# Optimization experiments

Hardware: AMD Instinct MI355X
Metric: run time of the kernel (lower is better)

Reference implementation:

```python
import jax, jax.numpy as jnp
import numpy as np

B, C, L, T = 8, 512, 2048, 64

def setup_inputs() -> dict:
    key = jax.random.key(0)
    k1, k2, k3 = jax.random.split(key, 3)
    x = jax.random.normal(k1, (B, C, 1, L), dtype=jnp.float32)
    W1 = jax.random.normal(k2, (T, C), dtype=jnp.float32) * (1.0 / np.sqrt(C))
    W2 = jax.random.normal(k3, (T, C), dtype=jnp.float32) * (1.0 / np.sqrt(C))
    gamma = jnp.ones((1, 1), dtype=jnp.float32)
    ranges = 0  # unused by forward
    return {"x": x, "W1": W1, "W2": W2, "gamma": gamma, "ranges": ranges}

def reference(x, W1, W2, gamma, ranges):
    temp = x[:, :, 0, :]                                  # (B, C, L)
    q = jnp.einsum('tc,bcl->btl', W1, temp)               # conv1x1 -> (B, T, L)
    k = jnp.einsum('tc,bcl->btl', W2, temp)               # conv1x1 -> (B, T, L)
    scores = jnp.einsum('btl,btm->blm', q, k)             # Q^T K -> (B, L, L)
    attn = jax.nn.softmax(scores, axis=2)                 # softmax over last dim
    # temp @ attn^T: out[:, :, j] = sum_i attn[j, i] * temp[:, :, i]
    out = jnp.einsum('bci,bji->bcj', temp, attn)          # (B, C, L)
    out = temp + gamma[0, 0] * out                        # gamma scale + residual
    return out[:, :, None, :]                             # (B, C, 1, L)
```

## Files before the change

### kernel.cpp

```cpp
#include <hip/hip_runtime.h>
#include <cstddef>

#define BB 8
#define CC 512
#define LL 2048
#define TT 64

typedef short short8 __attribute__((ext_vector_type(8)));
typedef float floatx4 __attribute__((ext_vector_type(4)));
typedef unsigned short b16u;
typedef unsigned int u32;

static __device__ __forceinline__ unsigned f2bfu(float f) {
    unsigned u = __float_as_uint(f);
    u += 0x7fffu + ((u >> 16) & 1u);
    return u >> 16;
}
static __device__ __forceinline__ float bfu2f(unsigned h) {
    return __uint_as_float(h << 16);
}

#define MFMA16(a, b, c) __builtin_amdgcn_mfma_f32_16x16x32_bf16((a), (b), (c), 0, 0, 0)

static __device__ __forceinline__ void gl2lds16(const void* g, void* l) {
    __builtin_amdgcn_global_load_lds(
        (const __attribute__((address_space(1))) u32*)g,
        (__attribute__((address_space(3))) u32*)l, 16, 0, 0);
}

__global__ __launch_bounds__(256) void wcvt_kernel(
    const float* __restrict__ W1, const float* __restrict__ W2,
    b16u* __restrict__ W1h, b16u* __restrict__ W1l,
    b16u* __restrict__ W2h, b16u* __restrict__ W2l)
{
    int flat = blockIdx.x * 256 + threadIdx.x;
    float4 v1 = *(const float4*)(W1 + (size_t)flat * 4);
    float4 v2 = *(const float4*)(W2 + (size_t)flat * 4);
    const float* e1 = (const float*)&v1;
    const float* e2 = (const float*)&v2;
    unsigned h1[4], l1[4], h2[4], l2[4];
#pragma unroll
    for (int k = 0; k < 4; ++k) {
        h1[k] = f2bfu(e1[k]); l1[k] = f2bfu(e1[k] - bfu2f(h1[k]));
        h2[k] = f2bfu(e2[k]); l2[k] = f2bfu(e2[k] - bfu2f(h2[k]));
    }
    uint2 a, b, c, d;
    a.x = h1[0] | (h1[1] << 16); a.y = h1[2] | (h1[3] << 16);
    b.x = l1[0] | (l1[1] << 16); b.y = l1[2] | (l1[3] << 16);
    c.x = h2[0] | (h2[1] << 16); c.y = h2[2] | (h2[3] << 16);
    d.x = l2[0] | (l2[1] << 16); d.y = l2[2] | (l2[3] << 16);
    *(uint2*)(W1h + (size_t)flat * 4) = a;
    *(uint2*)(W1l + (size_t)flat * 4) = b;
    *(uint2*)(W2h + (size_t)flat * 4) = c;
    *(uint2*)(W2l + (size_t)flat * 4) = d;
}

__global__ __launch_bounds__(256) void qkcvt_kernel(
    const float* __restrict__ x,
    const b16u* __restrict__ W1h, const b16u* __restrict__ W1l,
    const b16u* __restrict__ W2h, const b16u* __restrict__ W2l,
    b16u* __restrict__ Qt, b16u* __restrict__ Kt)
{
    __shared__ b16u Sxh[64 * 72];
    __shared__ b16u Sxl[64 * 72];
    __shared__ b16u S1h[64 * 72];
    __shared__ b16u S1l[64 * 72];
    __shared__ b16u S2h[64 * 72];
    __shared__ b16u S2l[64 * 72];
    const int b  = blockIdx.y;
    const int l0 = blockIdx.x * 64;
    const int tid = threadIdx.x;
    const int lane = tid & 63;
    const int w = tid >> 6;
    const int n16 = lane & 15;
    const int qd = lane >> 4;
    const float* xb = x + (size_t)b * CC * LL;

    const int cx = tid >> 2;
    const int sx = tid & 3;

    float4 xreg[4];
#pragma unroll
    for (int p = 0; p < 4; ++p)
        xreg[p] = *(const float4*)(xb + (size_t)cx * LL + l0 + (sx * 4 + p) * 4);

    floatx4 aq[4], ak[4];
#pragma unroll
    for (int nt = 0; nt < 4; ++nt) {
        aq[nt] = (floatx4){0.f, 0.f, 0.f, 0.f};
        ak[nt] = (floatx4){0.f, 0.f, 0.f, 0.f};
    }

    for (int c0 = 0; c0 < 512; c0 += 64) {
        __syncthreads();
#pragma unroll
        for (int p = 0; p < 4; ++p) {
            const float* e = (const float*)&xreg[p];
            int lbase = (sx * 4 + p) * 4;
#pragma unroll
            for (int k = 0; k < 4; ++k) {
                unsigned h = f2bfu(e[k]);
                unsigned lo = f2bfu(e[k] - bfu2f(h));
                Sxh[(lbase + k) * 72 + cx] = (b16u)h;
                Sxl[(lbase + k) * 72 + cx] = (b16u)lo;
            }
        }
#pragma unroll
        for (int p = 0; p < 2; ++p) {
            int flat = tid + p * 256;
            int t = flat >> 3, s8 = flat & 7;
            size_t off = (size_t)t * 512 + c0 + s8 * 8;
            *(uint4*)&S1h[t * 72 + s8 * 8] = *(const uint4*)(W1h + off);
            *(uint4*)&S1l[t * 72 + s8 * 8] = *(const uint4*)(W1l + off);
            *(uint4*)&S2h[t * 72 + s8 * 8] = *(const uint4*)(W2h + off);
            *(uint4*)&S2l[t * 72 + s8 * 8] = *(const uint4*)(W2l + off);
        }
        __syncthreads();
        if (c0 < 448) {
#pragma unroll
            for (int p = 0; p < 4; ++p)
                xreg[p] = *(const float4*)(xb + (size_t)(c0 + 64 + cx) * LL +
                                           l0 + (sx * 4 + p) * 4);
        }
#pragma unroll
        for (int kc = 0; kc < 2; ++kc) {
            const int ao = (w * 16 + n16) * 72 + kc * 32 + qd * 8;
            short8 a1h = *(const short8*)&S1h[ao];
            short8 a1l = *(const short8*)&S1l[ao];
            short8 a2h = *(const short8*)&S2h[ao];
            short8 a2l = *(const short8*)&S2l[ao];
#pragma unroll
            for (int nt = 0; nt < 4; ++nt) {
                const int bo = (nt * 16 + n16) * 72 + kc * 32 + qd * 8;
                short8 bh = *(const short8*)&Sxh[bo];
                short8 bl = *(const short8*)&Sxl[bo];
                aq[nt] = MFMA16(a1h, bh, aq[nt]);
                aq[nt] = MFMA16(a1h, bl, aq[nt]);
                aq[nt] = MFMA16(a1l, bh, aq[nt]);
                ak[nt] = MFMA16(a2h, bh, ak[nt]);
                ak[nt] = MFMA16(a2h, bl, ak[nt]);
                ak[nt] = MFMA16(a2l, bh, ak[nt]);
            }
        }
    }
#pragma unroll
    for (int nt = 0; nt < 4; ++nt) {
        int l = l0 + nt * 16 + n16;
        uint2 pq, pk;
        pq.x = f2bfu(aq[nt][0]) | (f2bfu(aq[nt][1]) << 16);
        pq.y = f2bfu(aq[nt][2]) | (f2bfu(aq[nt][3]) << 16);
        pk.x = f2bfu(ak[nt][0]) | (f2bfu(ak[nt][1]) << 16);
        pk.y = f2bfu(ak[nt][2]) | (f2bfu(ak[nt][3]) << 16);
        *(uint2*)(Qt + ((size_t)(b * 2048) + l) * 64 + w * 16 + qd * 4) = pq;
        *(uint2*)(Kt + ((size_t)(b * 2048) + l) * 64 + w * 16 + qd * 4) = pk;
    }
}

__global__ __launch_bounds__(256) void xcvt_kernel(
    const float* __restrict__ x, b16u* __restrict__ XT)
{
    const int b = blockIdx.z, c0 = blockIdx.y * 64, it = blockIdx.x;
    const int tid = threadIdx.x;
#pragma unroll
    for (int p = 0; p < 4; ++p) {
        int flat = tid + p * 256;
        int c = flat >> 4, s = flat & 15;
        float4 v = *(const float4*)(x + ((size_t)(b * 512) + c0 + c) * 2048 + it * 64 + s * 4);
        uint2 wv;
        wv.x = f2bfu(v.x) | (f2bfu(v.y) << 16);
        wv.y = f2bfu(v.z) | (f2bfu(v.w) << 16);
        int phys = (((s >> 1) ^ (c & 7)) << 3) + ((s & 1) << 2);
        *(uint2*)(XT + (((size_t)(b * 32) + it) * 512 + c0 + c) * 64 + phys) = wv;
    }
}

__global__ __launch_bounds__(256) void pexp_kernel(
    const b16u* __restrict__ Qt, const b16u* __restrict__ Kt,
    b16u* __restrict__ P, float* __restrict__ Zpart, int b_off)
{
    __shared__ b16u Ks[64 * 72];
    __shared__ b16u Ls[64 * 68];
    __shared__ float Zw[4][64];
    const int pb = blockIdx.z, b = b_off + pb;
    const int j0 = blockIdx.y * 64;
    const int ibase = blockIdx.x * 1024;
    const int tid = threadIdx.x;
    const int lane = tid & 63;
    const int w = tid >> 6;
    const int n16 = lane & 15;
    const int qd = lane >> 4;
    const b16u* kb = Kt + (size_t)b * (2048 * 64);

    short8 qf[4][2];
#pragma unroll
    for (int nt = 0; nt < 4; ++nt)
#pragma unroll
        for (int kc = 0; kc < 2; ++kc)
            qf[nt][kc] = *(const short8*)(Qt +
                ((size_t)(b * 2048) + j0 + nt * 16 + n16) * 64 + kc * 32 + qd * 8);

    uint4 kreg[2];
#pragma unroll
    for (int p = 0; p < 2; ++p) {
        int flat = tid + p * 256;
        kreg[p] = *(const uint4*)(kb + (size_t)(ibase + (flat >> 3)) * 64 + (flat & 7) * 8);
    }
    float zacc[4] = {0.f, 0.f, 0.f, 0.f};

    for (int it = 0; it < 16; ++it) {
#pragma unroll
        for (int p = 0; p < 2; ++p) {
            int flat = tid + p * 256;
            *(uint4*)&Ks[(flat >> 3) * 72 + (flat & 7) * 8] = kreg[p];
        }
        {
            const int itn = (it + 1 < 16) ? it + 1 : 15;
#pragma unroll
            for (int p = 0; p < 2; ++p) {
                int flat = tid + p * 256;
                kreg[p] = *(const uint4*)(kb +
                    (size_t)(ibase + itn * 64 + (flat >> 3)) * 64 + (flat & 7) * 8);
            }
        }
        __syncthreads();
        floatx4 sacc[4];
#pragma unroll
        for (int nt = 0; nt < 4; ++nt) sacc[nt] = (floatx4){0.f, 0.f, 0.f, 0.f};
#pragma unroll
        for (int kc = 0; kc < 2; ++kc) {
            short8 af = *(const short8*)&Ks[(w * 16 + n16) * 72 + kc * 32 + qd * 8];
#pragma unroll
            for (int nt = 0; nt < 4; ++nt)
                sacc[nt] = MFMA16(af, qf[nt][kc], sacc[nt]);
        }
#pragma unroll
        for (int nt = 0; nt < 4; ++nt) {
            float p0 = __expf(sacc[nt][0] - 20.0f);
            float p1 = __expf(sacc[nt][1] - 20.0f);
            float p2 = __expf(sacc[nt][2] - 20.0f);
            float p3 = __expf(sacc[nt][3] - 20.0f);
            zacc[nt] += (p0 + p1) + (p2 + p3);
            uint2 pk;
            pk.x = f2bfu(p0) | (f2bfu(p1) << 16);
            pk.y = f2bfu(p2) | (f2bfu(p3) << 16);
            *(uint2*)&Ls[(nt * 16 + n16) * 68 + w * 16 + qd * 4] = pk;
        }
        __syncthreads();
        size_t prow = ((size_t)(pb * 32) + (ibase >> 6) + it) * 2048 + j0;
#pragma unroll
        for (int p = 0; p < 4; ++p) {
            int u = tid + p * 256;
            int row = u >> 4, s = u & 15;
            int phys = (((s >> 1) ^ (row & 7)) << 3) + ((s & 1) << 2);
            *(uint2*)(P + (prow + row) * 64 + phys) = *(const uint2*)&Ls[row * 68 + s * 4];
        }
    }
#pragma unroll
    for (int nt = 0; nt < 4; ++nt) {
        float z = zacc[nt];
        z += __shfl_xor(z, 16);
        z += __shfl_xor(z, 32);
        if (qd == 0) Zw[w][nt * 16 + n16] = z;
    }
    __syncthreads();
    if (tid < 64) {
        float s = Zw[0][tid] + Zw[1][tid] + Zw[2][tid] + Zw[3][tid];
        Zpart[((size_t)blockIdx.x * 8 + b) * 2048 + j0 + tid] = s;
    }
}

__global__ __launch_bounds__(256, 2) void gemm_kernel(
    const float* __restrict__ x, const b16u* __restrict__ XT,
    const b16u* __restrict__ P, const float* __restrict__ Zpart,
    const float* __restrict__ gamma, float* __restrict__ out, int b_off)
{
    __shared__ __align__(16) char smem[69632];
    b16u* As = (b16u*)smem;
    b16u* Bs = (b16u*)(smem + 32768);
    const int pb = blockIdx.z, b = b_off + pb;
    const int j0 = blockIdx.x * 128;
    const int c0 = blockIdx.y * 128;
    const int tid = threadIdx.x;
    const int lane = tid & 63;
    const int w = tid >> 6;
    const int n16 = lane & 15;
    const int qd = lane >> 4;
    const int wc = w & 1;
    const int wj = w >> 1;

    const b16u* tA = XT + ((size_t)(b * 32) * 512 + c0) * 64 + w * 2048 + lane * 8;
    const b16u* tB = P + ((size_t)(pb * 32) * 2048 + j0) * 64 + w * 2048 + lane * 8;
    b16u* lA = As + w * 2048;
    b16u* lB = Bs + w * 2048;

#define STAGE(IT, BUF)                                                    \
    {                                                                      \
        const b16u* ga = tA + (size_t)(IT) * 32768;                        \
        const b16u* gb = tB + (size_t)(IT) * 131072;                       \
        _Pragma("unroll")                                                  \
        for (int ch = 0; ch < 4; ++ch) {                                   \
            gl2lds16(ga + ch * 512, lA + (BUF) * 8192 + ch * 512);         \
            gl2lds16(gb + ch * 512, lB + (BUF) * 8192 + ch * 512);         \
        }                                                                  \
    }

    STAGE(0, 0)
    __syncthreads();

    floatx4 acc[4][4];
#pragma unroll
    for (int mt = 0; mt < 4; ++mt)
#pragma unroll
        for (int nt = 0; nt < 4; ++nt) acc[mt][nt] = (floatx4){0.f, 0.f, 0.f, 0.f};

    for (int it = 0; it < 32; ++it) {
        const int buf = it & 1;
        if (it < 31) STAGE(it + 1, buf ^ 1)
        const b16u* Ab = As + buf * 8192;
        const b16u* Bb = Bs + buf * 8192;
#pragma unroll
        for (int kc = 0; kc < 2; ++kc) {
            const int co = (((kc * 4 + qd) ^ (n16 & 7)) << 3);
            short8 af[4], bf[4];
#pragma unroll
            for (int mt = 0; mt < 4; ++mt)
                af[mt] = *(const short8*)&Ab[(wc * 64 + mt * 16 + n16) * 64 + co];
#pragma unroll
            for (int nt = 0; nt < 4; ++nt)
                bf[nt] = *(const short8*)&Bb[(wj * 64 + nt * 16 + n16) * 64 + co];
#pragma unroll
            for (int mt = 0; mt < 4; ++mt)
#pragma unroll
                for (int nt = 0; nt < 4; ++nt)
                    acc[mt][nt] = MFMA16(af[mt], bf[nt], acc[mt][nt]);
        }
        __syncthreads();
    }
#undef STAGE

    const float g = gamma[0];
    float* st = (float*)(smem + w * 17408);
#pragma unroll
    for (int nt = 0; nt < 4; ++nt) {
        int j = j0 + wj * 64 + nt * 16 + n16;
        float zi = g / (Zpart[(size_t)b * 2048 + j] +
                        Zpart[16384 + (size_t)b * 2048 + j]);
#pragma unroll
        for (int mt = 0; mt < 4; ++mt)
#pragma unroll
            for (int r = 0; r < 4; ++r)
                st[(mt * 16 + qd * 4 + r) * 68 + nt * 16 + n16] = acc[mt][nt][r] * zi;
    }
    __syncthreads();
#pragma unroll
    for (int p = 0; p < 16; ++p) {
        int rl = qd * 16 + p;
        int cg = c0 + wc * 64 + rl;
        size_t go = ((size_t)(b * 512) + cg) * 2048 + j0 + wj * 64 + n16 * 4;
        float4 v = *(const float4*)&st[rl * 68 + n16 * 4];
        float4 xv = *(const float4*)(x + go);
        v.x += xv.x; v.y += xv.y; v.z += xv.z; v.w += xv.w;
        *(float4*)(out + go) = v;
    }
}

extern "C" void kernel_launch(void* const* d_in, const int* in_sizes, int n_in,
                              void* d_out, int out_size, void* d_ws, size_t ws_size,
                              hipStream_t stream)
{
    const float* x     = (const float*)d_in[0];
    const float* W1    = (const float*)d_in[1];
    const float* W2    = (const float*)d_in[2];
    const float* gamma = (const float*)d_in[3];
    float* out = (float*)d_out;

    b16u* Qt  = (b16u*)d_ws;
    b16u* Kt  = Qt  + (size_t)BB * LL * TT;
    b16u* W1h = Kt  + (size_t)BB * LL * TT;
    b16u* W1l = W1h + (size_t)TT * CC;
    b16u* W2h = W1l + (size_t)TT * CC;
    b16u* W2l = W2h + (size_t)TT * CC;
    float* Zp = (float*)(W2l + (size_t)TT * CC);
    b16u* XT  = (b16u*)(Zp + 2 * 8 * 2048);
    b16u* P   = XT + (size_t)BB * 32 * 512 * 64;

    const size_t base = (size_t)((char*)P - (char*)d_ws);
    const size_t pbat = (size_t)LL * LL * 2;
    int nb = 8;
    if (ws_size < base + 8 * pbat) nb = 4;
    if (ws_size < base + 4 * pbat) nb = 2;
    if (ws_size < base + 2 * pbat) nb = 1;

    wcvt_kernel <<<dim3(32),        256, 0, stream>>>(W1, W2, W1h, W1l, W2h, W2l);
    qkcvt_kernel<<<dim3(32, BB),    256, 0, stream>>>(x, W1h, W1l, W2h, W2l, Qt, Kt);
    xcvt_kernel <<<dim3(32, 8, BB), 256, 0, stream>>>(x, XT);
    for (int b0 = 0; b0 < BB; b0 += nb) {
        pexp_kernel<<<dim3(2, 32, nb), 256, 0, stream>>>(Qt, Kt, P, Zp, b0);
        gemm_kernel<<<dim3(16, 4, nb), 256, 0, stream>>>(x, XT, P, Zp, gamma, out, b0);
    }
}
```

Baseline: 177.5 us.

## Fuse score-exp and PV GEMM into one flash-style kernel, drop P buffer

Replaces the separate pexp and gemm kernels, which wrote and reread the full bf16 probability matrix (B×L×L) through global memory, with a single fused kernel. Each 512-thread block owns 64 query columns for all 512 channels, computes exp(scores) tiles into double-buffered LDS and immediately consumes them in MFMA against the bf16 x tile. Z normalization is reduced within the block. The x conversion becomes a plain linear transpose-free copy and V fragments are loaded straight from global. The cost is a grid of only 256 blocks with large LDS use and high register pressure, plus repeated global loads of x fragments per block without LDS staging.

```diff
diff --git a/kernel.cpp b/kernel.cpp
--- a/kernel.cpp
+++ b/kernel.cpp
@@ -21,12 +21,6 @@
 }
 
 #define MFMA16(a, b, c) __builtin_amdgcn_mfma_f32_16x16x32_bf16((a), (b), (c), 0, 0, 0)
-
-static __device__ __forceinline__ void gl2lds16(const void* g, void* l) {
-    __builtin_amdgcn_global_load_lds(
-        (const __attribute__((address_space(1))) u32*)g,
-        (__attribute__((address_space(3))) u32*)l, 16, 0, 0);
-}
 
 __global__ __launch_bounds__(256) void wcvt_kernel(
     const float* __restrict__ W1, const float* __restrict__ W2,
@@ -159,192 +153,140 @@
 __global__ __launch_bounds__(256) void xcvt_kernel(
     const float* __restrict__ x, b16u* __restrict__ XT)
 {
-    const int b = blockIdx.z, c0 = blockIdx.y * 64, it = blockIdx.x;
-    const int tid = threadIdx.x;
-#pragma unroll
-    for (int p = 0; p < 4; ++p) {
-        int flat = tid + p * 256;
-        int c = flat >> 4, s = flat & 15;
-        float4 v = *(const float4*)(x + ((size_t)(b * 512) + c0 + c) * 2048 + it * 64 + s * 4);
-        uint2 wv;
-        wv.x = f2bfu(v.x) | (f2bfu(v.y) << 16);
-        wv.y = f2bfu(v.z) | (f2bfu(v.w) << 16);
-        int phys = (((s >> 1) ^ (c & 7)) << 3) + ((s & 1) << 2);
-        *(uint2*)(XT + (((size_t)(b * 32) + it) * 512 + c0 + c) * 64 + phys) = wv;
-    }
-}
-
-__global__ __launch_bounds__(256) void pexp_kernel(
+    size_t idx = ((size_t)blockIdx.x * 256 + threadIdx.x) * 4;
+    float4 v = *(const float4*)(x + idx);
+    uint2 wv;
+    wv.x = f2bfu(v.x) | (f2bfu(v.y) << 16);
+    wv.y = f2bfu(v.z) | (f2bfu(v.w) << 16);
+    *(uint2*)(XT + idx) = wv;
+}
+
+__global__ __launch_bounds__(512, 2) void fused_kernel(
+    const float* __restrict__ x, const b16u* __restrict__ XT,
     const b16u* __restrict__ Qt, const b16u* __restrict__ Kt,
-    b16u* __restrict__ P, float* __restrict__ Zpart, int b_off)
-{
-    __shared__ b16u Ks[64 * 72];
-    __shared__ b16u Ls[64 * 68];
-    __shared__ float Zw[4][64];
-    const int pb = blockIdx.z, b = b_off + pb;
-    const int j0 = blockIdx.y * 64;
-    const int ibase = blockIdx.x * 1024;
+    const float* __restrict__ gamma, float* __restrict__ out)
+{
+    __shared__ __align__(16) char smem[139264 + 256];
+    b16u*  Pb = (b16u*)smem;
+    float* Zw = (float*)(smem + 16384);
+    float* Zf = (float*)(smem + 139264);
+
+    const int b   = blockIdx.x & 7;
+    const int j0  = (blockIdx.x >> 3) * 64;
     const int tid = threadIdx.x;
     const int lane = tid & 63;
-    const int w = tid >> 6;
-    const int n16 = lane & 15;
-    const int qd = lane >> 4;
-    const b16u* kb = Kt + (size_t)b * (2048 * 64);
-
-    short8 qf[4][2];
-#pragma unroll
-    for (int nt = 0; nt < 4; ++nt)
+    const int w    = tid >> 6;
+    const int n16  = lane & 15;
+    const int qd   = lane >> 4;
+    const int wi   = w & 3;
+    const int wj2  = w >> 2;
+
+    const b16u* Qb = Qt + ((size_t)(b * LL) + j0 + wj2 * 32 + n16) * 64 + qd * 8;
+    const b16u* Kb = Kt + ((size_t)(b * LL) + wi * 16 + n16) * 64 + qd * 8;
+    const b16u* Vb = XT + ((size_t)(b * CC) + w * 64 + n16) * 2048 + qd * 8;
+
+    short8 qf[2][2];
+#pragma unroll
+    for (int nt2 = 0; nt2 < 2; ++nt2)
 #pragma unroll
         for (int kc = 0; kc < 2; ++kc)
-            qf[nt][kc] = *(const short8*)(Qt +
-                ((size_t)(b * 2048) + j0 + nt * 16 + n16) * 64 + kc * 32 + qd * 8);
-
-    uint4 kreg[2];
-#pragma unroll
-    for (int p = 0; p < 2; ++p) {
-        int flat = tid + p * 256;
-        kreg[p] = *(const uint4*)(kb + (size_t)(ibase + (flat >> 3)) * 64 + (flat & 7) * 8);
-    }
-    float zacc[4] = {0.f, 0.f, 0.f, 0.f};
-
-    for (int it = 0; it < 16; ++it) {
-#pragma unroll
-        for (int p = 0; p < 2; ++p) {
-            int flat = tid + p * 256;
-            *(uint4*)&Ks[(flat >> 3) * 72 + (flat & 7) * 8] = kreg[p];
-        }
-        {
-            const int itn = (it + 1 < 16) ? it + 1 : 15;
-#pragma unroll
-            for (int p = 0; p < 2; ++p) {
-                int flat = tid + p * 256;
-                kreg[p] = *(const uint4*)(kb +
-                    (size_t)(ibase + itn * 64 + (flat >> 3)) * 64 + (flat & 7) * 8);
+            qf[nt2][kc] = *(const short8*)(Qb + nt2 * (16 * 64) + kc * 32);
+
+    floatx4 acc[4][4];
+#pragma unroll
+    for (int mt = 0; mt < 4; ++mt)
+#pragma unroll
+        for (int nt = 0; nt < 4; ++nt) acc[mt][nt] = (floatx4){0.f, 0.f, 0.f, 0.f};
+    float zacc[2] = {0.f, 0.f};
+
+#define S_STEP(BUFOFF, KF)                                                     \
+    {                                                                          \
+        _Pragma("unroll")                                                      \
+        for (int nt2 = 0; nt2 < 2; ++nt2) {                                    \
+            floatx4 sacc = (floatx4){0.f, 0.f, 0.f, 0.f};                      \
+            sacc = MFMA16(KF[0], qf[nt2][0], sacc);                            \
+            sacc = MFMA16(KF[1], qf[nt2][1], sacc);                            \
+            float p0 = __expf(sacc[0] - 20.0f);                                \
+            float p1 = __expf(sacc[1] - 20.0f);                                \
+            float p2 = __expf(sacc[2] - 20.0f);                                \
+            float p3 = __expf(sacc[3] - 20.0f);                                \
+            zacc[nt2] += (p0 + p1) + (p2 + p3);                                \
+            uint2 pk;                                                          \
+            pk.x = f2bfu(p0) | (f2bfu(p1) << 16);                              \
+            pk.y = f2bfu(p2) | (f2bfu(p3) << 16);                              \
+            int jl = wj2 * 32 + nt2 * 16 + n16;                                \
+            int phys = (wi * 2 + (qd >> 1)) ^ (jl & 7);                        \
+            *(uint2*)&Pb[(BUFOFF) + jl * 64 + phys * 8 + (qd & 1) * 4] = pk;   \
+        }                                                                      \
+    }
+
+    short8 kf[2];
+    kf[0] = *(const short8*)(Kb);
+    kf[1] = *(const short8*)(Kb + 32);
+    S_STEP(0, kf)
+    kf[0] = *(const short8*)(Kb + 64 * 64);
+    kf[1] = *(const short8*)(Kb + 64 * 64 + 32);
+    __syncthreads();
+
+    int buf = 0;
+    for (int t = 0; t < 32; ++t) {
+        short8 av[4][2];
+#pragma unroll
+        for (int mt = 0; mt < 4; ++mt)
+#pragma unroll
+            for (int kc = 0; kc < 2; ++kc)
+                av[mt][kc] = *(const short8*)(Vb + (size_t)mt * (16 * 2048) +
+                                              t * 64 + kc * 32);
+        if (t < 31) {
+            S_STEP((buf ^ 1) * 4096, kf)
+            if (t < 30) {
+                const b16u* kp = Kb + (size_t)(t + 2) * (64 * 64);
+                kf[0] = *(const short8*)(kp);
+                kf[1] = *(const short8*)(kp + 32);
             }
         }
+        __builtin_amdgcn_s_setprio(1);
+#pragma unroll
+        for (int kc = 0; kc < 2; ++kc) {
+            short8 bfr[4];
+#pragma unroll
+            for (int nt = 0; nt < 4; ++nt) {
+                int phys = (kc * 4 + qd) ^ (n16 & 7);
+                bfr[nt] = *(const short8*)&Pb[buf * 4096 +
+                                              (nt * 16 + n16) * 64 + phys * 8];
+            }
+#pragma unroll
+            for (int mt = 0; mt < 4; ++mt)
+#pragma unroll
+                for (int nt = 0; nt < 4; ++nt)
+                    acc[mt][nt] = MFMA16(av[mt][kc], bfr[nt], acc[mt][nt]);
+        }
+        __builtin_amdgcn_s_setprio(0);
         __syncthreads();
-        floatx4 sacc[4];
-#pragma unroll
-        for (int nt = 0; nt < 4; ++nt) sacc[nt] = (floatx4){0.f, 0.f, 0.f, 0.f};
-#pragma unroll
-        for (int kc = 0; kc < 2; ++kc) {
-            short8 af = *(const short8*)&Ks[(w * 16 + n16) * 72 + kc * 32 + qd * 8];
-#pragma unroll
-            for (int nt = 0; nt < 4; ++nt)
-                sacc[nt] = MFMA16(af, qf[nt][kc], sacc[nt]);
-        }
-#pragma unroll
-        for (int nt = 0; nt < 4; ++nt) {
-            float p0 = __expf(sacc[nt][0] - 20.0f);
-            float p1 = __expf(sacc[nt][1] - 20.0f);
-            float p2 = __expf(sacc[nt][2] - 20.0f);
-            float p3 = __expf(sacc[nt][3] - 20.0f);
-            zacc[nt] += (p0 + p1) + (p2 + p3);
-            uint2 pk;
-            pk.x = f2bfu(p0) | (f2bfu(p1) << 16);
-            pk.y = f2bfu(p2) | (f2bfu(p3) << 16);
-            *(uint2*)&Ls[(nt * 16 + n16) * 68 + w * 16 + qd * 4] = pk;
-        }
-        __syncthreads();
-        size_t prow = ((size_t)(pb * 32) + (ibase >> 6) + it) * 2048 + j0;
-#pragma unroll
-        for (int p = 0; p < 4; ++p) {
-            int u = tid + p * 256;
-            int row = u >> 4, s = u & 15;
-            int phys = (((s >> 1) ^ (row & 7)) << 3) + ((s & 1) << 2);
-            *(uint2*)(P + (prow + row) * 64 + phys) = *(const uint2*)&Ls[row * 68 + s * 4];
-        }
-    }
-#pragma unroll
-    for (int nt = 0; nt < 4; ++nt) {
-        float z = zacc[nt];
+        buf ^= 1;
+    }
+#undef S_STEP
+
+#pragma unroll
+    for (int nt2 = 0; nt2 < 2; ++nt2) {
+        float z = zacc[nt2];
         z += __shfl_xor(z, 16);
         z += __shfl_xor(z, 32);
-        if (qd == 0) Zw[w][nt * 16 + n16] = z;
+        if (qd == 0) Zw[w * 32 + nt2 * 16 + n16] = z;
     }
     __syncthreads();
     if (tid < 64) {
-        float s = Zw[0][tid] + Zw[1][tid] + Zw[2][tid] + Zw[3][tid];
-        Zpart[((size_t)blockIdx.x * 8 + b) * 2048 + j0 + tid] = s;
-    }
-}
-
-__global__ __launch_bounds__(256, 2) void gemm_kernel(
-    const float* __restrict__ x, const b16u* __restrict__ XT,
-    const b16u* __restrict__ P, const float* __restrict__ Zpart,
-    const float* __restrict__ gamma, float* __restrict__ out, int b_off)
-{
-    __shared__ __align__(16) char smem[69632];
-    b16u* As = (b16u*)smem;
-    b16u* Bs = (b16u*)(smem + 32768);
-    const int pb = blockIdx.z, b = b_off + pb;
-    const int j0 = blockIdx.x * 128;
-    const int c0 = blockIdx.y * 128;
-    const int tid = threadIdx.x;
-    const int lane = tid & 63;
-    const int w = tid >> 6;
-    const int n16 = lane & 15;
-    const int qd = lane >> 4;
-    const int wc = w & 1;
-    const int wj = w >> 1;
-
-    const b16u* tA = XT + ((size_t)(b * 32) * 512 + c0) * 64 + w * 2048 + lane * 8;
-    const b16u* tB = P + ((size_t)(pb * 32) * 2048 + j0) * 64 + w * 2048 + lane * 8;
-    b16u* lA = As + w * 2048;
-    b16u* lB = Bs + w * 2048;
-
-#define STAGE(IT, BUF)                                                    \
-    {                                                                      \
-        const b16u* ga = tA + (size_t)(IT) * 32768;                        \
-        const b16u* gb = tB + (size_t)(IT) * 131072;                       \
-        _Pragma("unroll")                                                  \
-        for (int ch = 0; ch < 4; ++ch) {                                   \
-            gl2lds16(ga + ch * 512, lA + (BUF) * 8192 + ch * 512);         \
-            gl2lds16(gb + ch * 512, lB + (BUF) * 8192 + ch * 512);         \
-        }                                                                  \
-    }
-
-    STAGE(0, 0)
+        int g2 = (tid >> 5) * 4;
+        Zf[tid] = Zw[(g2 + 0) * 32 + (tid & 31)] + Zw[(g2 + 1) * 32 + (tid & 31)] +
+                  Zw[(g2 + 2) * 32 + (tid & 31)] + Zw[(g2 + 3) * 32 + (tid & 31)];
+    }
     __syncthreads();
-
-    floatx4 acc[4][4];
-#pragma unroll
-    for (int mt = 0; mt < 4; ++mt)
-#pragma unroll
-        for (int nt = 0; nt < 4; ++nt) acc[mt][nt] = (floatx4){0.f, 0.f, 0.f, 0.f};
-
-    for (int it = 0; it < 32; ++it) {
-        const int buf = it & 1;
-        if (it < 31) STAGE(it + 1, buf ^ 1)
-        const b16u* Ab = As + buf * 8192;
-        const b16u* Bb = Bs + buf * 8192;
-#pragma unroll
-        for (int kc = 0; kc < 2; ++kc) {
-            const int co = (((kc * 4 + qd) ^ (n16 & 7)) << 3);
-            short8 af[4], bf[4];
-#pragma unroll
-            for (int mt = 0; mt < 4; ++mt)
-                af[mt] = *(const short8*)&Ab[(wc * 64 + mt * 16 + n16) * 64 + co];
-#pragma unroll
-            for (int nt = 0; nt < 4; ++nt)
-                bf[nt] = *(const short8*)&Bb[(wj * 64 + nt * 16 + n16) * 64 + co];
-#pragma unroll
-            for (int mt = 0; mt < 4; ++mt)
-#pragma unroll
-                for (int nt = 0; nt < 4; ++nt)
-                    acc[mt][nt] = MFMA16(af[mt], bf[nt], acc[mt][nt]);
-        }
-        __syncthreads();
-    }
-#undef STAGE
 
     const float g = gamma[0];
     float* st = (float*)(smem + w * 17408);
 #pragma unroll
     for (int nt = 0; nt < 4; ++nt) {
-        int j = j0 + wj * 64 + nt * 16 + n16;
-        float zi = g / (Zpart[(size_t)b * 2048 + j] +
-                        Zpart[16384 + (size_t)b * 2048 + j]);
+        float zi = g / Zf[nt * 16 + n16];
 #pragma unroll
         for (int mt = 0; mt < 4; ++mt)
 #pragma unroll
@@ -355,8 +297,7 @@
 #pragma unroll
     for (int p = 0; p < 16; ++p) {
         int rl = qd * 16 + p;
-        int cg = c0 + wc * 64 + rl;
-        size_t go = ((size_t)(b * 512) + cg) * 2048 + j0 + wj * 64 + n16 * 4;
+        size_t go = ((size_t)(b * CC) + w * 64 + rl) * 2048 + j0 + n16 * 4;
         float4 v = *(const float4*)&st[rl * 68 + n16 * 4];
         float4 xv = *(const float4*)(x + go);
         v.x += xv.x; v.y += xv.y; v.z += xv.z; v.w += xv.w;
@@ -368,6 +309,7 @@
                               void* d_out, int out_size, void* d_ws, size_t ws_size,
                               hipStream_t stream)
 {
+    (void)in_sizes; (void)n_in; (void)out_size; (void)ws_size;
     const float* x     = (const float*)d_in[0];
     const float* W1    = (const float*)d_in[1];
     const float* W2    = (const float*)d_in[2];
@@ -380,22 +322,10 @@
     b16u* W1l = W1h + (size_t)TT * CC;
     b16u* W2h = W1l + (size_t)TT * CC;
     b16u* W2l = W2h + (size_t)TT * CC;
-    float* Zp = (float*)(W2l + (size_t)TT * CC);
-    b16u* XT  = (b16u*)(Zp + 2 * 8 * 2048);
-    b16u* P   = XT + (size_t)BB * 32 * 512 * 64;
-
-    const size_t base = (size_t)((char*)P - (char*)d_ws);
-    const size_t pbat = (size_t)LL * LL * 2;
-    int nb = 8;
-    if (ws_size < base + 8 * pbat) nb = 4;
-    if (ws_size < base + 4 * pbat) nb = 2;
-    if (ws_size < base + 2 * pbat) nb = 1;
-
-    wcvt_kernel <<<dim3(32),        256, 0, stream>>>(W1, W2, W1h, W1l, W2h, W2l);
-    qkcvt_kernel<<<dim3(32, BB),    256, 0, stream>>>(x, W1h, W1l, W2h, W2l, Qt, Kt);
-    xcvt_kernel <<<dim3(32, 8, BB), 256, 0, stream>>>(x, XT);
-    for (int b0 = 0; b0 < BB; b0 += nb) {
-        pexp_kernel<<<dim3(2, 32, nb), 256, 0, stream>>>(Qt, Kt, P, Zp, b0);
-        gemm_kernel<<<dim3(16, 4, nb), 256, 0, stream>>>(x, XT, P, Zp, gamma, out, b0);
-    }
-}
+    b16u* XT  = W2l + (size_t)TT * CC;
+
+    wcvt_kernel <<<dim3(32),      256, 0, stream>>>(W1, W2, W1h, W1l, W2h, W2l);
+    xcvt_kernel <<<dim3(8192),    256, 0, stream>>>(x, XT);
+    qkcvt_kernel<<<dim3(32, BB),  256, 0, stream>>>(x, W1h, W1l, W2h, W2l, Qt, Kt);
+    fused_kernel<<<dim3(256),     512, 0, stream>>>(x, XT, Qt, Kt, gamma, out);
+}
```

After: 189.8 us. 6.9% more time.

## Replace split-bf16 MFMA Q/K projection with plain fp32 FMA kernel

Applied to the files above, without the earlier changes.

The Q/K projection no longer splits x and the weights into bf16 hi/lo parts and runs three MFMAs per product. It now uses a scalar fp32 FMA kernel: each thread owns one position l and 16 output channels, reading x coalesced and the transposed weights as broadcast loads with software double-buffering. The grid grows from 256 to 256 blocks of finer work (8 batches x 8 l-tiles x 4 t-quarters), with no LDS or syncs. This drops the conversion and LDS-staging overhead but gives up tensor-core throughput for about 0.5 GFLOP of projection work.

```diff
diff --git a/kernel.cpp b/kernel.cpp
--- a/kernel.cpp
+++ b/kernel.cpp
@@ -16,9 +16,6 @@
     u += 0x7fffu + ((u >> 16) & 1u);
     return u >> 16;
 }
-static __device__ __forceinline__ float bfu2f(unsigned h) {
-    return __uint_as_float(h << 16);
-}
 
 #define MFMA16(a, b, c) __builtin_amdgcn_mfma_f32_16x16x32_bf16((a), (b), (c), 0, 0, 0)
 
@@ -28,131 +25,76 @@
         (__attribute__((address_space(3))) u32*)l, 16, 0, 0);
 }
 
-__global__ __launch_bounds__(256) void wcvt_kernel(
+__global__ __launch_bounds__(256) void wprep_kernel(
     const float* __restrict__ W1, const float* __restrict__ W2,
-    b16u* __restrict__ W1h, b16u* __restrict__ W1l,
-    b16u* __restrict__ W2h, b16u* __restrict__ W2l)
+    float* __restrict__ WT1, float* __restrict__ WT2)
 {
     int flat = blockIdx.x * 256 + threadIdx.x;
-    float4 v1 = *(const float4*)(W1 + (size_t)flat * 4);
-    float4 v2 = *(const float4*)(W2 + (size_t)flat * 4);
-    const float* e1 = (const float*)&v1;
-    const float* e2 = (const float*)&v2;
-    unsigned h1[4], l1[4], h2[4], l2[4];
-#pragma unroll
-    for (int k = 0; k < 4; ++k) {
-        h1[k] = f2bfu(e1[k]); l1[k] = f2bfu(e1[k] - bfu2f(h1[k]));
-        h2[k] = f2bfu(e2[k]); l2[k] = f2bfu(e2[k] - bfu2f(h2[k]));
-    }
-    uint2 a, b, c, d;
-    a.x = h1[0] | (h1[1] << 16); a.y = h1[2] | (h1[3] << 16);
-    b.x = l1[0] | (l1[1] << 16); b.y = l1[2] | (l1[3] << 16);
-    c.x = h2[0] | (h2[1] << 16); c.y = h2[2] | (h2[3] << 16);
-    d.x = l2[0] | (l2[1] << 16); d.y = l2[2] | (l2[3] << 16);
-    *(uint2*)(W1h + (size_t)flat * 4) = a;
-    *(uint2*)(W1l + (size_t)flat * 4) = b;
-    *(uint2*)(W2h + (size_t)flat * 4) = c;
-    *(uint2*)(W2l + (size_t)flat * 4) = d;
-}
-
-__global__ __launch_bounds__(256) void qkcvt_kernel(
+    int c = flat >> 6, t = flat & 63;
+    WT1[flat] = W1[t * 512 + c];
+    WT2[flat] = W2[t * 512 + c];
+}
+
+__global__ __launch_bounds__(256, 4) void qk_kernel(
     const float* __restrict__ x,
-    const b16u* __restrict__ W1h, const b16u* __restrict__ W1l,
-    const b16u* __restrict__ W2h, const b16u* __restrict__ W2l,
+    const float* __restrict__ WT1, const float* __restrict__ WT2,
     b16u* __restrict__ Qt, b16u* __restrict__ Kt)
 {
-    __shared__ b16u Sxh[64 * 72];
-    __shared__ b16u Sxl[64 * 72];
-    __shared__ b16u S1h[64 * 72];
-    __shared__ b16u S1l[64 * 72];
-    __shared__ b16u S2h[64 * 72];
-    __shared__ b16u S2l[64 * 72];
-    const int b  = blockIdx.y;
-    const int l0 = blockIdx.x * 64;
-    const int tid = threadIdx.x;
-    const int lane = tid & 63;
-    const int w = tid >> 6;
-    const int n16 = lane & 15;
-    const int qd = lane >> 4;
-    const float* xb = x + (size_t)b * CC * LL;
-
-    const int cx = tid >> 2;
-    const int sx = tid & 3;
-
-    float4 xreg[4];
-#pragma unroll
-    for (int p = 0; p < 4; ++p)
-        xreg[p] = *(const float4*)(xb + (size_t)cx * LL + l0 + (sx * 4 + p) * 4);
-
-    floatx4 aq[4], ak[4];
-#pragma unroll
-    for (int nt = 0; nt < 4; ++nt) {
-        aq[nt] = (floatx4){0.f, 0.f, 0.f, 0.f};
-        ak[nt] = (floatx4){0.f, 0.f, 0.f, 0.f};
-    }
-
-    for (int c0 = 0; c0 < 512; c0 += 64) {
-        __syncthreads();
-#pragma unroll
-        for (int p = 0; p < 4; ++p) {
-            const float* e = (const float*)&xreg[p];
-            int lbase = (sx * 4 + p) * 4;
-#pragma unroll
-            for (int k = 0; k < 4; ++k) {
-                unsigned h = f2bfu(e[k]);
-                unsigned lo = f2bfu(e[k] - bfu2f(h));
-                Sxh[(lbase + k) * 72 + cx] = (b16u)h;
-                Sxl[(lbase + k) * 72 + cx] = (b16u)lo;
-            }
-        }
-#pragma unroll
-        for (int p = 0; p < 2; ++p) {
-            int flat = tid + p * 256;
-            int t = flat >> 3, s8 = flat & 7;
-            size_t off = (size_t)t * 512 + c0 + s8 * 8;
-            *(uint4*)&S1h[t * 72 + s8 * 8] = *(const uint4*)(W1h + off);
-            *(uint4*)&S1l[t * 72 + s8 * 8] = *(const uint4*)(W1l + off);
-            *(uint4*)&S2h[t * 72 + s8 * 8] = *(const uint4*)(W2h + off);
-            *(uint4*)&S2l[t * 72 + s8 * 8] = *(const uint4*)(W2l + off);
-        }
-        __syncthreads();
-        if (c0 < 448) {
-#pragma unroll
-            for (int p = 0; p < 4; ++p)
-                xreg[p] = *(const float4*)(xb + (size_t)(c0 + 64 + cx) * LL +
-                                           l0 + (sx * 4 + p) * 4);
-        }
-#pragma unroll
-        for (int kc = 0; kc < 2; ++kc) {
-            const int ao = (w * 16 + n16) * 72 + kc * 32 + qd * 8;
-            short8 a1h = *(const short8*)&S1h[ao];
-            short8 a1l = *(const short8*)&S1l[ao];
-            short8 a2h = *(const short8*)&S2h[ao];
-            short8 a2l = *(const short8*)&S2l[ao];
-#pragma unroll
-            for (int nt = 0; nt < 4; ++nt) {
-                const int bo = (nt * 16 + n16) * 72 + kc * 32 + qd * 8;
-                short8 bh = *(const short8*)&Sxh[bo];
-                short8 bl = *(const short8*)&Sxl[bo];
-                aq[nt] = MFMA16(a1h, bh, aq[nt]);
-                aq[nt] = MFMA16(a1h, bl, aq[nt]);
-                aq[nt] = MFMA16(a1l, bh, aq[nt]);
-                ak[nt] = MFMA16(a2h, bh, ak[nt]);
-                ak[nt] = MFMA16(a2h, bl, ak[nt]);
-                ak[nt] = MFMA16(a2l, bh, ak[nt]);
-            }
-        }
-    }
-#pragma unroll
-    for (int nt = 0; nt < 4; ++nt) {
-        int l = l0 + nt * 16 + n16;
-        uint2 pq, pk;
-        pq.x = f2bfu(aq[nt][0]) | (f2bfu(aq[nt][1]) << 16);
-        pq.y = f2bfu(aq[nt][2]) | (f2bfu(aq[nt][3]) << 16);
-        pk.x = f2bfu(ak[nt][0]) | (f2bfu(ak[nt][1]) << 16);
-        pk.y = f2bfu(ak[nt][2]) | (f2bfu(ak[nt][3]) << 16);
-        *(uint2*)(Qt + ((size_t)(b * 2048) + l) * 64 + w * 16 + qd * 4) = pq;
-        *(uint2*)(Kt + ((size_t)(b * 2048) + l) * 64 + w * 16 + qd * 4) = pk;
+    const int bid = blockIdx.x;
+    const int b  = bid & 7;
+    const int lt = (bid >> 3) & 7;
+    const int tq = bid >> 6;
+    const int l  = lt * 256 + threadIdx.x;
+    const float* xb = x + (size_t)b * CC * LL + l;
+    const float* w1 = WT1 + tq * 16;
+    const float* w2 = WT2 + tq * 16;
+
+    float qa[16], ka[16];
+#pragma unroll
+    for (int t = 0; t < 16; ++t) { qa[t] = 0.f; ka[t] = 0.f; }
+
+    float4 wqA[4], wkA[4], wqB[4], wkB[4];
+    float xA, xB;
+
+#define QKLOAD(WQ, WK, XV, C)                                              \
+    {                                                                      \
+        const float* p1 = w1 + (size_t)(C) * 64;                           \
+        const float* p2 = w2 + (size_t)(C) * 64;                           \
+        WQ[0] = *(const float4*)(p1);                                      \
+        WQ[1] = *(const float4*)(p1 + 4);                                  \
+        WQ[2] = *(const float4*)(p1 + 8);                                  \
+        WQ[3] = *(const float4*)(p1 + 12);                                 \
+        WK[0] = *(const float4*)(p2);                                      \
+        WK[1] = *(const float4*)(p2 + 4);                                  \
+        WK[2] = *(const float4*)(p2 + 8);                                  \
+        WK[3] = *(const float4*)(p2 + 12);                                 \
+        XV = xb[(size_t)(C) * LL];                                         \
+    }
+#define QKFMA(WQ, WK, XV)                                                  \
+    {                                                                      \
+        _Pragma("unroll")                                                  \
+        for (int t = 0; t < 16; ++t) {                                     \
+            qa[t] += ((const float*)&WQ[t >> 2])[t & 3] * XV;              \
+            ka[t] += ((const float*)&WK[t >> 2])[t & 3] * XV;              \
+        }                                                                  \
+    }
+
+    QKLOAD(wqA, wkA, xA, 0)
+    for (int c = 0; c < 512; c += 2) {
+        if (c + 1 < 512) QKLOAD(wqB, wkB, xB, c + 1)
+        QKFMA(wqA, wkA, xA)
+        if (c + 2 < 512) QKLOAD(wqA, wkA, xA, c + 2)
+        QKFMA(wqB, wkB, xB)
+    }
+#undef QKLOAD
+#undef QKFMA
+
+    b16u* qo = Qt + ((size_t)(b * LL) + l) * 64 + tq * 16;
+    b16u* ko = Kt + ((size_t)(b * LL) + l) * 64 + tq * 16;
+#pragma unroll
+    for (int p = 0; p < 8; ++p) {
+        *(u32*)(qo + p * 2) = f2bfu(qa[p * 2]) | (f2bfu(qa[p * 2 + 1]) << 16);
+        *(u32*)(ko + p * 2) = f2bfu(ka[p * 2]) | (f2bfu(ka[p * 2 + 1]) << 16);
     }
 }
 
@@ -368,21 +310,20 @@
                               void* d_out, int out_size, void* d_ws, size_t ws_size,
                               hipStream_t stream)
 {
+    (void)in_sizes; (void)n_in; (void)out_size;
     const float* x     = (const float*)d_in[0];
     const float* W1    = (const float*)d_in[1];
     const float* W2    = (const float*)d_in[2];
     const float* gamma = (const float*)d_in[3];
     float* out = (float*)d_out;
 
-    b16u* Qt  = (b16u*)d_ws;
-    b16u* Kt  = Qt  + (size_t)BB * LL * TT;
-    b16u* W1h = Kt  + (size_t)BB * LL * TT;
-    b16u* W1l = W1h + (size_t)TT * CC;
-    b16u* W2h = W1l + (size_t)TT * CC;
-    b16u* W2l = W2h + (size_t)TT * CC;
-    float* Zp = (float*)(W2l + (size_t)TT * CC);
-    b16u* XT  = (b16u*)(Zp + 2 * 8 * 2048);
-    b16u* P   = XT + (size_t)BB * 32 * 512 * 64;
+    b16u*  Qt  = (b16u*)d_ws;
+    b16u*  Kt  = Qt + (size_t)BB * LL * TT;
+    float* WT1 = (float*)(Kt + (size_t)BB * LL * TT);
+    float* WT2 = WT1 + (size_t)TT * CC;
+    float* Zp  = WT2 + (size_t)TT * CC;
+    b16u*  XT  = (b16u*)(Zp + 2 * 8 * 2048);
+    b16u*  P   = XT + (size_t)BB * 32 * 512 * 64;
 
     const size_t base = (size_t)((char*)P - (char*)d_ws);
     const size_t pbat = (size_t)LL * LL * 2;
@@ -391,8 +332,8 @@
     if (ws_size < base + 4 * pbat) nb = 2;
     if (ws_size < base + 2 * pbat) nb = 1;
 
-    wcvt_kernel <<<dim3(32),        256, 0, stream>>>(W1, W2, W1h, W1l, W2h, W2l);
-    qkcvt_kernel<<<dim3(32, BB),    256, 0, stream>>>(x, W1h, W1l, W2h, W2l, Qt, Kt);
+    wprep_kernel<<<dim3(128),       256, 0, stream>>>(W1, W2, WT1, WT2);
+    qk_kernel   <<<dim3(256),       256, 0, stream>>>(x, WT1, WT2, Qt, Kt);
     xcvt_kernel <<<dim3(32, 8, BB), 256, 0, stream>>>(x, XT);
     for (int b0 = 0; b0 < BB; b0 += nb) {
         pexp_kernel<<<dim3(2, 32, nb), 256, 0, stream>>>(Qt, Kt, P, Zp, b0);
```

Result: slower. 421.8 us (+137.7%).
